# Kernel optimization log

Measured on AMD Instinct MI355X. Metric: run time of the kernel, lower is better.

Reference implementation:

```python
import jax, jax.numpy as jnp
import numpy as np

MARGIN = 0.3

def _pairwise_euclid(x):
    # torch.cdist(x, x, p=2): [N, N] Euclidean distances, zero-safe sqrt
    sq_norms = jnp.sum(x * x, axis=1)                       # [N]
    sq = sq_norms[:, None] + sq_norms[None, :] - 2.0 * (x @ x.T)
    sq = jnp.maximum(sq, 0.0)
    safe = jnp.where(sq > 0.0, sq, 1.0)
    return jnp.where(sq > 0.0, jnp.sqrt(safe), 0.0)

def setup_inputs() -> dict:
    key = jax.random.key(0)
    k1, k2 = jax.random.split(key)
    features = jax.random.normal(k1, (4096, 512), dtype=jnp.float32)
    labels = jax.random.randint(k2, (4096,), 0, 256, dtype=jnp.int64)
    return {"features": features, "labels": labels}

def reference(features, labels):
    n = features.shape[0]
    dist = _pairwise_euclid(features)                       # [N, N]
    pos_mask = labels[:, None] == labels[None, :]           # includes self
    neg_inf = jnp.float32(-np.inf)
    pos_inf = jnp.float32(np.inf)
    hardest_pos = jnp.max(jnp.where(pos_mask, dist, neg_inf), axis=1)   # [N]
    hardest_neg = jnp.min(jnp.where(pos_mask, pos_inf, dist), axis=1)   # [N]
    valid = jnp.sum(pos_mask, axis=1) > 1                   # >1 positives incl. self
    per_row = jax.nn.relu(hardest_pos - hardest_neg + MARGIN)
    loss = jnp.sum(jnp.where(valid, per_row, 0.0)) / n
    return loss
```

## Files before the change

kernel.cpp:

```cpp
#include <hip/hip_runtime.h>

#define NROWS 4096
#define DIM   512
#define MARGIN 0.3f

typedef _Float16 f16;
typedef _Float16 f16x8 __attribute__((ext_vector_type(8)));
typedef float    f32x4 __attribute__((ext_vector_type(4)));

__global__ void norms_init_kernel(const float* __restrict__ X,
                                  float* __restrict__ norms,
                                  unsigned* __restrict__ hp, unsigned* __restrict__ hn) {
    int wave = threadIdx.x >> 6;
    int lane = threadIdx.x & 63;
    int row  = blockIdx.x * 4 + wave;
    const float4* xr = (const float4*)(X + (size_t)row * DIM);
    float4 a = xr[lane];
    float4 b = xr[lane + 64];
    float s = a.x*a.x + a.y*a.y + a.z*a.z + a.w*a.w
            + b.x*b.x + b.y*b.y + b.z*b.z + b.w*b.w;
    #pragma unroll
    for (int o = 32; o; o >>= 1) s += __shfl_xor(s, o);
    if (lane == 0) norms[row] = s;
    int g = blockIdx.x * 256 + threadIdx.x;
    if (g < NROWS) { hp[g] = 0u; hn[g] = 0x7f800000u; }
}

__global__ void convert_kernel(const float* __restrict__ X, f16* __restrict__ Xh) {
    int g = blockIdx.x * 256 + threadIdx.x;
    int tile = g >> 9, u = g & 511;
    int R = tile >> 4, K0 = tile & 15;
    int rg = u >> 6, c = (u >> 4) & 3, r = u & 15;
    int row = R * 128 + rg * 16 + r;
    int k0  = K0 * 32 + c * 8;
    const float4* p = (const float4*)(X + (size_t)row * DIM + k0);
    float4 a = p[0], b = p[1];
    f16x8 h;
    h[0] = (f16)a.x; h[1] = (f16)a.y; h[2] = (f16)a.z; h[3] = (f16)a.w;
    h[4] = (f16)b.x; h[5] = (f16)b.y; h[6] = (f16)b.z; h[7] = (f16)b.w;
    *(f16x8*)(Xh + (size_t)g * 8) = h;
}

__device__ inline void gload_lds16(const f16* g, f16* l) {
    __builtin_amdgcn_global_load_lds(
        (const __attribute__((address_space(1))) void*)g,
        (__attribute__((address_space(3))) void*)l, 16, 0, 0);
}

__device__ inline void stage_tile(const f16* __restrict__ At, const f16* __restrict__ Bt,
                                  f16* buf, int qb, int lane) {
    const f16* base = (qb < 512) ? (At + (size_t)qb * 8) : (Bt + (size_t)(qb - 512) * 8);
    #pragma unroll
    for (int c2 = 0; c2 < 4; ++c2)
        gload_lds16(base + (size_t)(c2 * 64 + lane) * 8, buf + (size_t)(qb + c2 * 64) * 8);
}

__global__ __launch_bounds__(256, 3) void mfma_dist_kernel(
        const f16* __restrict__ Xh, const int* __restrict__ labels,
        const float* __restrict__ norms,
        unsigned* __restrict__ hp, unsigned* __restrict__ hn) {
    __shared__ __align__(16) f16 S0[8192];
    __shared__ __align__(16) f16 S1[8192];

    const int t    = threadIdx.x;
    const int lane = t & 63, w = t >> 6;
    const int l15  = lane & 15, l4 = lane >> 4;

    int bt = blockIdx.x;
    int bx = (int)((sqrtf(8.0f * bt + 1.0f) - 1.0f) * 0.5f);
    while ((bx + 1) * (bx + 2) / 2 <= bt) ++bx;
    while (bx * (bx + 1) / 2 > bt) --bx;
    int by = bt - bx * (bx + 1) / 2;

    const int wr = w >> 1, wc = w & 1;
    const int qb = w * 256;

    const f16* Abase = Xh + (size_t)(by * 16) * 4096;
    const f16* Bbase = Xh + (size_t)(bx * 16) * 4096;

    f32x4 zero = {0.f, 0.f, 0.f, 0.f};
    f32x4 acc[4][4];
    #pragma unroll
    for (int m = 0; m < 4; ++m)
        #pragma unroll
        for (int n = 0; n < 4; ++n) acc[m][n] = zero;

    stage_tile(Abase, Bbase, S0, qb, lane);
    __syncthreads();

    #pragma unroll
    for (int kt = 0; kt < 16; ++kt) {
        f16* cur = (kt & 1) ? S1 : S0;
        f16* nxt = (kt & 1) ? S0 : S1;
        if (kt < 15)
            stage_tile(Abase + (size_t)(kt + 1) * 4096,
                       Bbase + (size_t)(kt + 1) * 4096, nxt, qb, lane);
        f16x8 af[4], bf[4];
        #pragma unroll
        for (int m = 0; m < 4; ++m)
            af[m] = *(const f16x8*)&cur[(size_t)((wr * 4 + m) * 64 + l4 * 16 + l15) * 8];
        #pragma unroll
        for (int n = 0; n < 4; ++n)
            bf[n] = *(const f16x8*)&cur[(size_t)(512 + (wc * 4 + n) * 64 + l4 * 16 + l15) * 8];
        #pragma unroll
        for (int m = 0; m < 4; ++m)
            #pragma unroll
            for (int n = 0; n < 4; ++n)
                acc[m][n] = __builtin_amdgcn_mfma_f32_16x16x32_f16(af[m], bf[n], acc[m][n], 0, 0, 0);
        if (kt < 15) __syncthreads();
    }

    const int wrow = by * 128 + wr * 64;
    const int wcol = bx * 128 + wc * 64;
    const float FINF = __uint_as_float(0x7f800000u);

    int lj[4]; float nj[4];
    #pragma unroll
    for (int n = 0; n < 4; ++n) {
        int gc = wcol + n * 16 + l15; lj[n] = labels[gc]; nj[n] = norms[gc];
    }
    int li[16]; float ni[16];
    #pragma unroll
    for (int m = 0; m < 4; ++m)
        #pragma unroll
        for (int r = 0; r < 4; ++r) {
            int gr = wrow + m * 16 + l4 * 4 + r;
            li[m * 4 + r] = labels[gr]; ni[m * 4 + r] = norms[gr];
        }

    float cp[4], cn[4];
    #pragma unroll
    for (int n = 0; n < 4; ++n) { cp[n] = 0.f; cn[n] = FINF; }

    #pragma unroll
    for (int m = 0; m < 4; ++m) {
        #pragma unroll
        for (int r = 0; r < 4; ++r) {
            float rp = 0.f, rn = FINF;
            #pragma unroll
            for (int n = 0; n < 4; ++n) {
                float sq = fmaxf(fmaf(-2.f, acc[m][n][r], ni[m * 4 + r] + nj[n]), 0.f);
                bool same = (li[m * 4 + r] == lj[n]);
                rp = same ? fmaxf(rp, sq) : rp;
                rn = same ? rn : fminf(rn, sq);
                cp[n] = same ? fmaxf(cp[n], sq) : cp[n];
                cn[n] = same ? cn[n] : fminf(cn[n], sq);
            }
            #pragma unroll
            for (int o = 8; o; o >>= 1) {
                rp = fmaxf(rp, __shfl_xor(rp, o));
                rn = fminf(rn, __shfl_xor(rn, o));
            }
            if (l15 == 0) {
                int gr = wrow + m * 16 + l4 * 4 + r;
                atomicMax(&hp[gr], __float_as_uint(rp));
                atomicMin(&hn[gr], __float_as_uint(rn));
            }
        }
    }
    #pragma unroll
    for (int n = 0; n < 4; ++n) {
        float p = cp[n], q = cn[n];
        p = fmaxf(p, __shfl_xor(p, 16)); q = fminf(q, __shfl_xor(q, 16));
        p = fmaxf(p, __shfl_xor(p, 32)); q = fminf(q, __shfl_xor(q, 32));
        if (l4 == 0) {
            int gc = wcol + n * 16 + l15;
            atomicMax(&hp[gc], __float_as_uint(p));
            atomicMin(&hn[gc], __float_as_uint(q));
        }
    }
}

#define BK  32
#define PAD 68
__global__ __launch_bounds__(256) void dist_fp32_kernel(
        const float* __restrict__ X, const int* __restrict__ labels,
        const float* __restrict__ norms,
        unsigned* __restrict__ hp, unsigned* __restrict__ hn) {
    __shared__ __align__(16) float As[BK][PAD];
    __shared__ __align__(16) float Bs[BK][PAD];
    const int t  = threadIdx.x;
    const int tx = t & 15, ty = t >> 4;
    const int row0 = blockIdx.y * 64, col0 = blockIdx.x * 64;

    float acc[4][4] = {};
    for (int k0 = 0; k0 < DIM; k0 += BK) {
        #pragma unroll
        for (int l = 0; l < 2; ++l) {
            int idx = t + l * 256;
            int r = idx >> 3, fc = idx & 7;
            float4 va = *(const float4*)(X + (size_t)(row0 + r) * DIM + k0 + fc * 4);
            float4 vb = *(const float4*)(X + (size_t)(col0 + r) * DIM + k0 + fc * 4);
            As[fc*4+0][r] = va.x; As[fc*4+1][r] = va.y;
            As[fc*4+2][r] = va.z; As[fc*4+3][r] = va.w;
            Bs[fc*4+0][r] = vb.x; Bs[fc*4+1][r] = vb.y;
            Bs[fc*4+2][r] = vb.z; Bs[fc*4+3][r] = vb.w;
        }
        __syncthreads();
        #pragma unroll
        for (int kk = 0; kk < BK; ++kk) {
            float4 a = *(const float4*)&As[kk][ty * 4];
            float4 b = *(const float4*)&Bs[kk][tx * 4];
            float av[4] = {a.x, a.y, a.z, a.w};
            float bv[4] = {b.x, b.y, b.z, b.w};
            #pragma unroll
            for (int m = 0; m < 4; ++m)
                #pragma unroll
                for (int n = 0; n < 4; ++n)
                    acc[m][n] = fmaf(av[m], bv[n], acc[m][n]);
        }
        __syncthreads();
    }
    int li[4], lj[4]; float ni[4], nj[4];
    #pragma unroll
    for (int m = 0; m < 4; ++m) {
        int gi = row0 + ty * 4 + m; li[m] = labels[gi]; ni[m] = norms[gi];
    }
    #pragma unroll
    for (int n = 0; n < 4; ++n) {
        int gj = col0 + tx * 4 + n; lj[n] = labels[gj]; nj[n] = norms[gj];
    }
    #pragma unroll
    for (int m = 0; m < 4; ++m) {
        float pmax = 0.0f;
        float nmin = __uint_as_float(0x7f800000u);
        #pragma unroll
        for (int n = 0; n < 4; ++n) {
            float sq = fmaxf(ni[m] + nj[n] - 2.0f * acc[m][n], 0.0f);
            if (li[m] == lj[n]) pmax = fmaxf(pmax, sq);
            else                nmin = fminf(nmin, sq);
        }
        #pragma unroll
        for (int o = 8; o; o >>= 1) {
            pmax = fmaxf(pmax, __shfl_xor(pmax, o));
            nmin = fminf(nmin, __shfl_xor(nmin, o));
        }
        if (tx == 0) {
            int gi = row0 + ty * 4 + m;
            atomicMax(&hp[gi], __float_as_uint(pmax));
            atomicMin(&hn[gi], __float_as_uint(nmin));
        }
    }
}

__global__ __launch_bounds__(1024) void finalize_kernel(
        const unsigned* __restrict__ hp, const unsigned* __restrict__ hn,
        const int* __restrict__ labels, float* __restrict__ out) {
    __shared__ int hist[256];
    __shared__ float wsum[16];
    int t = threadIdx.x;
    if (t < 256) hist[t] = 0;
    __syncthreads();
    int4 lab = ((const int4*)labels)[t];
    atomicAdd(&hist[lab.x], 1); atomicAdd(&hist[lab.y], 1);
    atomicAdd(&hist[lab.z], 1); atomicAdd(&hist[lab.w], 1);
    __syncthreads();
    uint4 hp4 = ((const uint4*)hp)[t];
    uint4 hn4 = ((const uint4*)hn)[t];
    int      lv[4]  = {lab.x, lab.y, lab.z, lab.w};
    unsigned hpv[4] = {hp4.x, hp4.y, hp4.z, hp4.w};
    unsigned hnv[4] = {hn4.x, hn4.y, hn4.z, hn4.w};
    float v = 0.f;
    #pragma unroll
    for (int j = 0; j < 4; ++j) {
        float hpd = sqrtf(__uint_as_float(hpv[j]));
        float hnd = sqrtf(__uint_as_float(hnv[j]));
        if (hist[lv[j]] > 1) v += fmaxf(hpd - hnd + MARGIN, 0.f);
    }
    #pragma unroll
    for (int o = 32; o; o >>= 1) v += __shfl_xor(v, o);
    int lane = t & 63, wv = t >> 6;
    if (lane == 0) wsum[wv] = v;
    __syncthreads();
    if (t == 0) {
        float s = 0.f;
        #pragma unroll
        for (int i = 0; i < 16; ++i) s += wsum[i];
        out[0] = s / (float)NROWS;
    }
}

extern "C" void kernel_launch(void* const* d_in, const int* in_sizes, int n_in,
                              void* d_out, int out_size, void* d_ws, size_t ws_size,
                              hipStream_t stream) {
    const float* X      = (const float*)d_in[0];
    const int*   labels = (const int*)d_in[1];
    float* ws = (float*)d_ws;
    float*    norms = ws;
    unsigned* hp    = (unsigned*)(ws + 4096);
    unsigned* hn    = (unsigned*)(ws + 8192);
    f16*      Xh    = (f16*)((char*)d_ws + 65536);
    float*    out   = (float*)d_out;

    const size_t need = 65536 + (size_t)NROWS * DIM * sizeof(f16);

    hipLaunchKernelGGL(norms_init_kernel, dim3(NROWS/4), dim3(256), 0, stream, X, norms, hp, hn);
    if (ws_size >= need) {
        hipLaunchKernelGGL(convert_kernel,   dim3(1024), dim3(256), 0, stream, X, Xh);
        hipLaunchKernelGGL(mfma_dist_kernel, dim3(528),  dim3(256), 0, stream, Xh, labels, norms, hp, hn);
    } else {
        hipLaunchKernelGGL(dist_fp32_kernel, dim3(64, 64), dim3(256), 0, stream, X, labels, norms, hp, hn);
    }
    hipLaunchKernelGGL(finalize_kernel, dim3(1), dim3(1024), 0, stream, hp, hn, labels, out);
}
```

Before: 41.56 us.

## Fuse norms/convert into one prep kernel and finalize into last GEMM block

Merges the norm computation, hp/hn init and fp16 tiled conversion into a single prep kernel that reads X once. The separate finalize kernel is folded into the MFMA distance kernel: the last block to finish, detected with an atomic counter, computes the label histogram and the reduction. This cuts the kernel launches from four to two and removes a redundant read of X. In exchange, the last block runs the serial finalize tail, and correctness depends on the fence and counter ordering.

```diff
diff --git a/kernel.cpp b/kernel.cpp
--- a/kernel.cpp
+++ b/kernel.cpp
@@ -8,37 +8,32 @@
 typedef _Float16 f16x8 __attribute__((ext_vector_type(8)));
 typedef float    f32x4 __attribute__((ext_vector_type(4)));
 
-__global__ void norms_init_kernel(const float* __restrict__ X,
-                                  float* __restrict__ norms,
-                                  unsigned* __restrict__ hp, unsigned* __restrict__ hn) {
-    int wave = threadIdx.x >> 6;
-    int lane = threadIdx.x & 63;
+__global__ void prep_kernel(const float* __restrict__ X,
+                            float* __restrict__ norms, f16* __restrict__ Xh,
+                            unsigned* __restrict__ hp, unsigned* __restrict__ hn,
+                            unsigned* __restrict__ cnt) {
+    int t = threadIdx.x;
+    int wave = t >> 6, lane = t & 63;
     int row  = blockIdx.x * 4 + wave;
-    const float4* xr = (const float4*)(X + (size_t)row * DIM);
-    float4 a = xr[lane];
-    float4 b = xr[lane + 64];
+    const float4* p = (const float4*)(X + (size_t)row * DIM + lane * 8);
+    float4 a = p[0], b = p[1];
     float s = a.x*a.x + a.y*a.y + a.z*a.z + a.w*a.w
             + b.x*b.x + b.y*b.y + b.z*b.z + b.w*b.w;
     #pragma unroll
     for (int o = 32; o; o >>= 1) s += __shfl_xor(s, o);
     if (lane == 0) norms[row] = s;
-    int g = blockIdx.x * 256 + threadIdx.x;
-    if (g < NROWS) { hp[g] = 0u; hn[g] = 0x7f800000u; }
-}
-
-__global__ void convert_kernel(const float* __restrict__ X, f16* __restrict__ Xh) {
-    int g = blockIdx.x * 256 + threadIdx.x;
-    int tile = g >> 9, u = g & 511;
-    int R = tile >> 4, K0 = tile & 15;
-    int rg = u >> 6, c = (u >> 4) & 3, r = u & 15;
-    int row = R * 128 + rg * 16 + r;
-    int k0  = K0 * 32 + c * 8;
-    const float4* p = (const float4*)(X + (size_t)row * DIM + k0);
-    float4 a = p[0], b = p[1];
+
     f16x8 h;
     h[0] = (f16)a.x; h[1] = (f16)a.y; h[2] = (f16)a.z; h[3] = (f16)a.w;
     h[4] = (f16)b.x; h[5] = (f16)b.y; h[6] = (f16)b.z; h[7] = (f16)b.w;
-    *(f16x8*)(Xh + (size_t)g * 8) = h;
+    int K0 = lane >> 2, c = lane & 3;
+    int R = row >> 7, rw = row & 127, rg = rw >> 4, r = rw & 15;
+    size_t unit = (size_t)(R * 16 + K0) * 512 + rg * 64 + c * 16 + r;
+    *(f16x8*)(Xh + unit * 8) = h;
+
+    int g = blockIdx.x * 256 + t;
+    if (g < NROWS) { hp[g] = 0u; hn[g] = 0x7f800000u; }
+    if (g == 0) *cnt = 0u;
 }
 
 __device__ inline void gload_lds16(const f16* g, f16* l) {
@@ -58,9 +53,11 @@
 __global__ __launch_bounds__(256, 3) void mfma_dist_kernel(
         const f16* __restrict__ Xh, const int* __restrict__ labels,
         const float* __restrict__ norms,
-        unsigned* __restrict__ hp, unsigned* __restrict__ hn) {
+        unsigned* __restrict__ hp, unsigned* __restrict__ hn,
+        unsigned* __restrict__ cnt, float* __restrict__ out) {
     __shared__ __align__(16) f16 S0[8192];
     __shared__ __align__(16) f16 S1[8192];
+    __shared__ int lastflag;
 
     const int t    = threadIdx.x;
     const int lane = t & 63, w = t >> 6;
@@ -169,6 +166,60 @@
             atomicMin(&hn[gc], __float_as_uint(q));
         }
     }
+
+    __threadfence();
+    if (t == 0) lastflag = (atomicAdd(cnt, 1u) == gridDim.x - 1) ? 1 : 0;
+    __syncthreads();
+    if (lastflag == 0) return;
+
+    int* hist = (int*)S0;
+    hist[t] = 0;
+    __syncthreads();
+    {
+        const int4* lab4 = (const int4*)labels;
+        #pragma unroll
+        for (int jj = 0; jj < 4; ++jj) {
+            int4 lb = lab4[t * 4 + jj];
+            atomicAdd(&hist[lb.x], 1); atomicAdd(&hist[lb.y], 1);
+            atomicAdd(&hist[lb.z], 1); atomicAdd(&hist[lb.w], 1);
+        }
+    }
+    __syncthreads();
+    float v = 0.f;
+    #pragma unroll
+    for (int j = 0; j < 16; ++j) {
+        int i = j * 256 + t;
+        unsigned hpv = __hip_atomic_load(&hp[i], __ATOMIC_RELAXED, __HIP_MEMORY_SCOPE_AGENT);
+        unsigned hnv = __hip_atomic_load(&hn[i], __ATOMIC_RELAXED, __HIP_MEMORY_SCOPE_AGENT);
+        if (hist[labels[i]] > 1) {
+            float d = sqrtf(__uint_as_float(hpv)) - sqrtf(__uint_as_float(hnv)) + MARGIN;
+            v += fmaxf(d, 0.f);
+        }
+    }
+    #pragma unroll
+    for (int o = 32; o; o >>= 1) v += __shfl_xor(v, o);
+    float* wsum = (float*)(S0 + 512);
+    if ((t & 63) == 0) wsum[t >> 6] = v;
+    __syncthreads();
+    if (t == 0) out[0] = (wsum[0] + wsum[1] + wsum[2] + wsum[3]) / (float)NROWS;
+}
+
+__global__ void norms_init_kernel(const float* __restrict__ X,
+                                  float* __restrict__ norms,
+                                  unsigned* __restrict__ hp, unsigned* __restrict__ hn) {
+    int wave = threadIdx.x >> 6;
+    int lane = threadIdx.x & 63;
+    int row  = blockIdx.x * 4 + wave;
+    const float4* xr = (const float4*)(X + (size_t)row * DIM);
+    float4 a = xr[lane];
+    float4 b = xr[lane + 64];
+    float s = a.x*a.x + a.y*a.y + a.z*a.z + a.w*a.w
+            + b.x*b.x + b.y*b.y + b.z*b.z + b.w*b.w;
+    #pragma unroll
+    for (int o = 32; o; o >>= 1) s += __shfl_xor(s, o);
+    if (lane == 0) norms[row] = s;
+    int g = blockIdx.x * 256 + threadIdx.x;
+    if (g < NROWS) { hp[g] = 0u; hn[g] = 0x7f800000u; }
 }
 
 #define BK  32
@@ -289,17 +340,20 @@
     float*    norms = ws;
     unsigned* hp    = (unsigned*)(ws + 4096);
     unsigned* hn    = (unsigned*)(ws + 8192);
+    unsigned* cnt   = (unsigned*)(ws + 12288);
     f16*      Xh    = (f16*)((char*)d_ws + 65536);
     float*    out   = (float*)d_out;
 
     const size_t need = 65536 + (size_t)NROWS * DIM * sizeof(f16);
 
-    hipLaunchKernelGGL(norms_init_kernel, dim3(NROWS/4), dim3(256), 0, stream, X, norms, hp, hn);
     if (ws_size >= need) {
-        hipLaunchKernelGGL(convert_kernel,   dim3(1024), dim3(256), 0, stream, X, Xh);
-        hipLaunchKernelGGL(mfma_dist_kernel, dim3(528),  dim3(256), 0, stream, Xh, labels, norms, hp, hn);
+        hipLaunchKernelGGL(prep_kernel, dim3(NROWS/4), dim3(256), 0, stream,
+                           X, norms, Xh, hp, hn, cnt);
+        hipLaunchKernelGGL(mfma_dist_kernel, dim3(528), dim3(256), 0, stream,
+                           Xh, labels, norms, hp, hn, cnt, out);
     } else {
+        hipLaunchKernelGGL(norms_init_kernel, dim3(NROWS/4), dim3(256), 0, stream, X, norms, hp, hn);
         hipLaunchKernelGGL(dist_fp32_kernel, dim3(64, 64), dim3(256), 0, stream, X, labels, norms, hp, hn);
-    }
-    hipLaunchKernelGGL(finalize_kernel, dim3(1), dim3(1024), 0, stream, hp, hn, labels, out);
-}
+        hipLaunchKernelGGL(finalize_kernel, dim3(1), dim3(1024), 0, stream, hp, hn, labels, out);
+    }
+}
```

New measurement: 63.96 us. 53.9% more time.
